# Optimization experiments

Measured on AMD Instinct MI355X. Metric: run time of the kernel, lower is better.

Reference implementation:

```python
import jax, jax.numpy as jnp
import numpy as np

D_MODEL = 1024
N_HEAD = 16
D_HEAD = 64
QLEN = 1024
KLEN = 2048
BSZ = 4


def _rel_shift(x):
    # x: [q, r, b, n]. TXL rel-shift: zero-pad along dim 1, view with first two
    # dims swapped (flat-buffer reshape, NOT transpose), drop first row, view back.
    q, r, b, n = x.shape
    zero_pad = jnp.zeros((q, 1, b, n), dtype=x.dtype)
    x_padded = jnp.concatenate([zero_pad, x], axis=1)  # [q, r+1, b, n]
    x_padded = x_padded.reshape(r + 1, q, b, n)
    return x_padded[1:].reshape(q, r, b, n)


def setup_inputs() -> dict:
    key = jax.random.key(0)
    ks = jax.random.split(key, 6)
    scale = 0.02
    return {
        "w_head_q": jax.random.normal(ks[0], (QLEN, BSZ, N_HEAD, D_HEAD), jnp.float32),
        "w_head_k": jax.random.normal(ks[1], (KLEN, BSZ, N_HEAD, D_HEAD), jnp.float32),
        "r": jax.random.normal(ks[2], (KLEN, D_MODEL), jnp.float32),
        "W_r": jax.random.normal(ks[3], (N_HEAD * D_HEAD, D_MODEL), jnp.float32) * scale,
        "r_w_bias": jax.random.normal(ks[4], (N_HEAD, D_HEAD), jnp.float32) * scale,
        "r_r_bias": jax.random.normal(ks[5], (N_HEAD, D_HEAD), jnp.float32) * scale,
        "rlen": KLEN,
    }


def reference(w_head_q, w_head_k, r, W_r, r_w_bias, r_r_bias, rlen):
    # r_net: Linear(d_model -> n_head*d_head, bias=False)
    r_head_k = (r @ W_r.T).reshape(rlen, N_HEAD, D_HEAD)  # [r, n, d]
    # C: content bias term, [1, klen, 1, n]
    C = jnp.einsum('nd,jbnd->jn', r_w_bias, w_head_k)[None, :, None, :]
    # B: query x rel-pos keys, [q, r, b, n]
    B = jnp.einsum('ibnd,jnd->ijbn', w_head_q, r_head_k)
    # D: position bias term, [1, r, 1, n]
    D = jnp.einsum('nd,jnd->jn', r_r_bias, r_head_k)[None, :, None, :]
    BD = _rel_shift(B + D)
    return C + BD
```

## Files before the change

kernel.cpp:

```cpp
#include <hip/hip_runtime.h>

#define QLEN 1024
#define KLEN 2048
#define BSZ 4
#define NHEAD 16
#define DHEAD 64
#define DMODEL 1024
#define RP1 2049

typedef short short8 __attribute__((ext_vector_type(8)));
typedef short short4v __attribute__((ext_vector_type(4)));
typedef float float4v __attribute__((ext_vector_type(4)));

__device__ inline float bf2f(unsigned short u) {
    union { unsigned int i; float f; } v; v.i = ((unsigned int)u) << 16; return v.f;
}
__device__ inline unsigned short f2bf(float f) {
    union { float f; unsigned int i; } v; v.f = f;
    unsigned int x = v.i;
    return (unsigned short)((x + 0x7fffu + ((x >> 16) & 1u)) >> 16);
}

__global__ __launch_bounds__(256) void conv_q(const float4v* __restrict__ in,
                                              short4v* __restrict__ outp, int n4) {
    int idx = blockIdx.x * 256 + threadIdx.x;
    if (idx < n4) {
        float4v v = in[idx];
        short4v s;
        s[0] = (short)f2bf(v[0]); s[1] = (short)f2bf(v[1]);
        s[2] = (short)f2bf(v[2]); s[3] = (short)f2bf(v[3]);
        outp[idx] = s;
    }
}

__global__ __launch_bounds__(256) void rk_gemm(const float* __restrict__ r,
                                               const float* __restrict__ wr,
                                               unsigned short* __restrict__ rk) {
    int tid = threadIdx.x;
    int w = tid >> 6, lane = tid & 63, li = lane & 15, quad = lane >> 4;
    int m0 = blockIdx.x * 64 + (w & 1) * 32;
    int n0 = blockIdx.y * 64 + (w >> 1) * 32;
    float4v acc[2][2] = {};
    for (int kk = 0; kk < DMODEL; kk += 32) {
        short8 a[2], b[2];
#pragma unroll
        for (int t = 0; t < 2; ++t) {
            const float* ap = r  + (size_t)(m0 + t*16 + li) * DMODEL + kk + quad*8;
            const float* bp = wr + (size_t)(n0 + t*16 + li) * DMODEL + kk + quad*8;
            float4v a0 = *(const float4v*)ap, a1 = *(const float4v*)(ap + 4);
            float4v b0 = *(const float4v*)bp, b1 = *(const float4v*)(bp + 4);
#pragma unroll
            for (int j = 0; j < 4; ++j) {
                a[t][j]   = (short)f2bf(a0[j]); a[t][j+4] = (short)f2bf(a1[j]);
                b[t][j]   = (short)f2bf(b0[j]); b[t][j+4] = (short)f2bf(b1[j]);
            }
        }
#pragma unroll
        for (int mi = 0; mi < 2; ++mi)
#pragma unroll
            for (int ni = 0; ni < 2; ++ni)
                acc[mi][ni] = __builtin_amdgcn_mfma_f32_16x16x32_bf16(a[mi], b[ni], acc[mi][ni], 0, 0, 0);
    }
#pragma unroll
    for (int mi = 0; mi < 2; ++mi)
#pragma unroll
        for (int ni = 0; ni < 2; ++ni)
#pragma unroll
            for (int rr = 0; rr < 4; ++rr) {
                int m = m0 + mi*16 + quad*4 + rr;
                int n = n0 + ni*16 + li;
                rk[(size_t)m * DMODEL + n] = f2bf(acc[mi][ni][rr]);
            }
}

__global__ __launch_bounds__(256) void c_kernel(const float* __restrict__ k,
                                                const float* __restrict__ bw,
                                                float* __restrict__ C) {
    int idx = blockIdx.x * 256 + threadIdx.x;
    int j = idx >> 4, n = idx & 15;
    float acc = 0.f;
#pragma unroll
    for (int b = 0; b < BSZ; ++b) {
        const float4v* kp = (const float4v*)(k + (size_t)j * 4096 + b * 1024 + n * 64);
        const float4v* wp = (const float4v*)(bw + n * 64);
#pragma unroll
        for (int d4 = 0; d4 < 16; ++d4) {
            float4v kv = kp[d4], wv = wp[d4];
            acc += wv[0]*kv[0] + wv[1]*kv[1] + wv[2]*kv[2] + wv[3]*kv[3];
        }
    }
    C[idx] = acc;
}

__global__ __launch_bounds__(256) void d_kernel(const unsigned short* __restrict__ rk,
                                                const float* __restrict__ br,
                                                float* __restrict__ D) {
    int idx = blockIdx.x * 256 + threadIdx.x;
    int kpos = idx >> 4, n = idx & 15;
    const unsigned short* rp = rk + (size_t)kpos * DMODEL + n * 64;
    float acc = 0.f;
#pragma unroll
    for (int d = 0; d < 64; ++d)
        acc += br[n*64 + d] * bf2f(rp[d]);
    D[idx] = acc;
}

__global__ __launch_bounds__(256) void gap_kernel(const float* __restrict__ C,
                                                  float* __restrict__ out) {
    int idx = blockIdx.x * 256 + threadIdx.x;
    if (idx >= 1023 * 64) return;
    int i = idx >> 6, c = idx & 63;
    int f = i * RP1 + 1025;
    int j = f & 2047;
    int n = c & 15;
    out[(size_t)f * 64 + c] = C[j * 16 + n];
}

__global__ __launch_bounds__(256) void main_kernel(const unsigned short* __restrict__ qb,
                                                   const unsigned short* __restrict__ rkb,
                                                   const float* __restrict__ Cp,
                                                   const float* __restrict__ Dp,
                                                   float* __restrict__ out) {
    __shared__ float lds[16 * 16 * 64];
    int tid = threadIdx.x;
    int w = tid >> 6, lane = tid & 63, li = lane & 15, quad = lane >> 4;
    int i0 = blockIdx.x * 16;
    int kb = blockIdx.y * 16;
    int k = kb + li;
    const unsigned short* qbase = qb + (size_t)(i0 + li) * 4096 + w * 16 * 64 + quad * 8;
    const unsigned short* rbase = rkb + (size_t)k * DMODEL + quad * 8;
    for (int n = 0; n < 16; ++n) {
        short8 a0 = *(const short8*)(qbase + n * 64);
        short8 a1 = *(const short8*)(qbase + n * 64 + 32);
        short8 b0 = *(const short8*)(rbase + n * 64);
        short8 b1 = *(const short8*)(rbase + n * 64 + 32);
        float4v acc = {0.f, 0.f, 0.f, 0.f};
        acc = __builtin_amdgcn_mfma_f32_16x16x32_bf16(a0, b0, acc, 0, 0, 0);
        acc = __builtin_amdgcn_mfma_f32_16x16x32_bf16(a1, b1, acc, 0, 0, 0);
        float dv = Dp[k * 16 + n];
        int c = w * 16 + n;
        int csw = c ^ ((li & 7) << 2) ^ quad;
#pragma unroll
        for (int rr = 0; rr < 4; ++rr) {
            int iloc = quad * 4 + rr;
            int f = (i0 + iloc) * RP1 + k - 1023;
            int j = f & 2047;
            lds[(iloc * 16 + li) * 64 + csw] = acc[rr] + dv + Cp[j * 16 + n];
        }
    }
    __syncthreads();
    int kloc = tid >> 4;
    int c0 = (tid & 15) * 4;
    int kx = (kloc & 7) << 2;
#pragma unroll
    for (int il = 0; il < 16; ++il) {
        int f = (i0 + il) * RP1 + kb + kloc - 1023;
        if (f >= 0) {
            int qx = (il >> 2) & 3;
            const float4v L = *(const float4v*)&lds[(il * 16 + kloc) * 64 + (c0 ^ kx)];
            float4v v;
            v[0] = L[0 ^ qx]; v[1] = L[1 ^ qx]; v[2] = L[2 ^ qx]; v[3] = L[3 ^ qx];
            *(float4v*)(out + (size_t)f * 64 + c0) = v;
        }
    }
}

extern "C" void kernel_launch(void* const* d_in, const int* in_sizes, int n_in,
                              void* d_out, int out_size, void* d_ws, size_t ws_size,
                              hipStream_t stream) {
    const float* q  = (const float*)d_in[0];
    const float* k  = (const float*)d_in[1];
    const float* r  = (const float*)d_in[2];
    const float* wr = (const float*)d_in[3];
    const float* bw = (const float*)d_in[4];
    const float* br = (const float*)d_in[5];
    float* out = (float*)d_out;

    unsigned short* rk = (unsigned short*)d_ws;
    unsigned short* qbf = (unsigned short*)((char*)d_ws + (4u << 20));
    float* C = (float*)((char*)d_ws + (12u << 20));
    float* D = (float*)((char*)d_ws + (12u << 20) + (128u << 10));

    conv_q<<<4096, 256, 0, stream>>>((const float4v*)q, (short4v*)qbf, QLEN * BSZ * NHEAD * DHEAD / 4);
    rk_gemm<<<dim3(KLEN / 64, DMODEL / 64), 256, 0, stream>>>(r, wr, rk);
    c_kernel<<<(KLEN * NHEAD) / 256, 256, 0, stream>>>(k, bw, C);
    d_kernel<<<(KLEN * NHEAD) / 256, 256, 0, stream>>>(rk, br, D);
    gap_kernel<<<(1023 * 64 + 255) / 256, 256, 0, stream>>>(C, out);
    main_kernel<<<dim3(QLEN / 16, KLEN / 16), 256, 0, stream>>>(qbf, rk, C, D, out);
}
```

Baseline: 836.4 us.

## Remap main kernel blocks per XCD, prefetch operands, use nontemporal output stores

Flattens the main kernel grid and remaps block IDs so each XCD works on a contiguous group of query tiles, with the goal of improving L2 reuse of q and rk tiles. Software-prefetches the next head's MFMA operands and C/D values one iteration ahead and precomputes the C row pointers. Output stores in the main and gap kernels become nontemporal so the large write stream does not pollute the caches. Prefetching raises register pressure, and the remap assumes the hardware assigns blocks to XCDs round-robin.

```diff
diff --git a/kernel.cpp b/kernel.cpp
--- a/kernel.cpp
+++ b/kernel.cpp
@@ -113,7 +113,7 @@
     int f = i * RP1 + 1025;
     int j = f & 2047;
     int n = c & 15;
-    out[(size_t)f * 64 + c] = C[j * 16 + n];
+    __builtin_nontemporal_store(C[j * 16 + n], out + (size_t)f * 64 + c);
 }
 
 __global__ __launch_bounds__(256) void main_kernel(const unsigned short* __restrict__ qb,
@@ -124,28 +124,55 @@
     __shared__ float lds[16 * 16 * 64];
     int tid = threadIdx.x;
     int w = tid >> 6, lane = tid & 63, li = lane & 15, quad = lane >> 4;
-    int i0 = blockIdx.x * 16;
-    int kb = blockIdx.y * 16;
+
+    int bid = blockIdx.x;
+    int xcd = bid & 7;
+    int r2 = bid >> 3;
+    int i_tile = xcd * 8 + (r2 & 7);
+    int kb = (r2 >> 3) * 16;
+    int i0 = i_tile * 16;
+
     int k = kb + li;
     const unsigned short* qbase = qb + (size_t)(i0 + li) * 4096 + w * 16 * 64 + quad * 8;
     const unsigned short* rbase = rkb + (size_t)k * DMODEL + quad * 8;
+
+    const float* crow[4];
+#pragma unroll
+    for (int rr = 0; rr < 4; ++rr)
+        crow[rr] = Cp + (((i0 + quad * 4 + rr + k - 1023) & 2047) << 4);
+    const float* drow = Dp + k * 16;
+
+    short8 a0 = *(const short8*)(qbase);
+    short8 a1 = *(const short8*)(qbase + 32);
+    short8 b0 = *(const short8*)(rbase);
+    short8 b1 = *(const short8*)(rbase + 32);
+    float dv = drow[0];
+    float cv0 = crow[0][0], cv1 = crow[1][0], cv2 = crow[2][0], cv3 = crow[3][0];
+
     for (int n = 0; n < 16; ++n) {
-        short8 a0 = *(const short8*)(qbase + n * 64);
-        short8 a1 = *(const short8*)(qbase + n * 64 + 32);
-        short8 b0 = *(const short8*)(rbase + n * 64);
-        short8 b1 = *(const short8*)(rbase + n * 64 + 32);
+        short8 na0, na1, nb0, nb1;
+        float ndv, ncv0, ncv1, ncv2, ncv3;
+        if (n < 15) {
+            const unsigned short* qn = qbase + (n + 1) * 64;
+            const unsigned short* rn = rbase + (n + 1) * 64;
+            na0 = *(const short8*)qn;  na1 = *(const short8*)(qn + 32);
+            nb0 = *(const short8*)rn;  nb1 = *(const short8*)(rn + 32);
+            ndv = drow[n + 1];
+            ncv0 = crow[0][n + 1]; ncv1 = crow[1][n + 1];
+            ncv2 = crow[2][n + 1]; ncv3 = crow[3][n + 1];
+        }
         float4v acc = {0.f, 0.f, 0.f, 0.f};
         acc = __builtin_amdgcn_mfma_f32_16x16x32_bf16(a0, b0, acc, 0, 0, 0);
         acc = __builtin_amdgcn_mfma_f32_16x16x32_bf16(a1, b1, acc, 0, 0, 0);
-        float dv = Dp[k * 16 + n];
         int c = w * 16 + n;
         int csw = c ^ ((li & 7) << 2) ^ quad;
-#pragma unroll
-        for (int rr = 0; rr < 4; ++rr) {
-            int iloc = quad * 4 + rr;
-            int f = (i0 + iloc) * RP1 + k - 1023;
-            int j = f & 2047;
-            lds[(iloc * 16 + li) * 64 + csw] = acc[rr] + dv + Cp[j * 16 + n];
+        lds[((quad * 4 + 0) * 16 + li) * 64 + csw] = (acc[0] + dv) + cv0;
+        lds[((quad * 4 + 1) * 16 + li) * 64 + csw] = (acc[1] + dv) + cv1;
+        lds[((quad * 4 + 2) * 16 + li) * 64 + csw] = (acc[2] + dv) + cv2;
+        lds[((quad * 4 + 3) * 16 + li) * 64 + csw] = (acc[3] + dv) + cv3;
+        if (n < 15) {
+            a0 = na0; a1 = na1; b0 = nb0; b1 = nb1;
+            dv = ndv; cv0 = ncv0; cv1 = ncv1; cv2 = ncv2; cv3 = ncv3;
         }
     }
     __syncthreads();
@@ -160,7 +187,7 @@
             const float4v L = *(const float4v*)&lds[(il * 16 + kloc) * 64 + (c0 ^ kx)];
             float4v v;
             v[0] = L[0 ^ qx]; v[1] = L[1 ^ qx]; v[2] = L[2 ^ qx]; v[3] = L[3 ^ qx];
-            *(float4v*)(out + (size_t)f * 64 + c0) = v;
+            __builtin_nontemporal_store(v, (float4v*)(out + (size_t)f * 64 + c0));
         }
     }
 }
@@ -186,5 +213,5 @@
     c_kernel<<<(KLEN * NHEAD) / 256, 256, 0, stream>>>(k, bw, C);
     d_kernel<<<(KLEN * NHEAD) / 256, 256, 0, stream>>>(rk, br, D);
     gap_kernel<<<(1023 * 64 + 255) / 256, 256, 0, stream>>>(C, out);
-    main_kernel<<<dim3(QLEN / 16, KLEN / 16), 256, 0, stream>>>(qbf, rk, C, D, out);
-}
+    main_kernel<<<8192, 256, 0, stream>>>(qbf, rk, C, D, out);
+}
```

After: 826.3 us. No clear change (-1.2%).
